# Kernel tuning notes

Measured on AMD Instinct MI355X. Metric: run time of the kernel, lower is better.

Reference implementation:

```python
import jax, jax.numpy as jnp
import numpy as np
from jax import lax

KH, KW, K = 3, 3, 9
PAD, BN_EPS = 1, 1e-5


def setup_inputs() -> dict:
    key = jax.random.key(0)
    ks = jax.random.split(key, 10)
    B, CHI, CHO, H, W = 2, 64, 64, 128, 128
    x = jax.random.normal(ks[0], (B, CHI, H, W), dtype=jnp.float32)
    # offset/mask branch conv: 3*K output channels (o1, o2, mask)
    w_off = jax.random.normal(ks[1], (3 * K, CHI, KH, KW), dtype=jnp.float32) * 0.01
    b_off = jax.random.normal(ks[2], (3 * K,), dtype=jnp.float32) * 0.01
    # main deformable conv weight/bias
    fan = CHI * K
    weight = jax.random.normal(ks[3], (CHO, CHI, KH, KW), dtype=jnp.float32) / np.sqrt(fan)
    bias = jax.random.normal(ks[4], (CHO,), dtype=jnp.float32) * 0.01
    # BatchNorm (eval-mode) params
    gamma = jax.random.uniform(ks[5], (CHO,), minval=0.5, maxval=1.5, dtype=jnp.float32)
    beta = jax.random.normal(ks[6], (CHO,), dtype=jnp.float32) * 0.1
    run_mean = jax.random.normal(ks[7], (CHO,), dtype=jnp.float32) * 0.1
    run_var = jax.random.uniform(ks[8], (CHO,), minval=0.5, maxval=1.5, dtype=jnp.float32)
    return {"x": x, "w_off": w_off, "b_off": b_off, "weight": weight,
            "bias": bias, "gamma": gamma, "beta": beta,
            "run_mean": run_mean, "run_var": run_var}


def _dcn_bn_relu(x, w_off, b_off, weight, bias, gamma, beta, run_mean, run_var):
    B, C, H, W = x.shape
    CHO = weight.shape[0]
    # offset/mask branch: regular 3x3 conv, stride 1, pad 1
    om = lax.conv_general_dilated(
        x, w_off, window_strides=(1, 1), padding=[(PAD, PAD), (PAD, PAD)],
        dimension_numbers=("NCHW", "OIHW", "NCHW")) + b_off[None, :, None, None]
    o1, o2, m = jnp.split(om, 3, axis=1)          # each [B, K, H, W]
    offset = jnp.concatenate([o1, o2], axis=1)    # [B, 2K, H, W]
    off_y = offset[:, 0::2]                       # interleaved (y, x) per tap, as in DCNv2 CUDA
    off_x = offset[:, 1::2]
    mask = jax.nn.sigmoid(m)                      # [B, K, H, W] modulation

    # sampling positions: p = p0 + p_k + offset
    ky, kx = jnp.meshgrid(jnp.arange(KH), jnp.arange(KW), indexing="ij")
    ky = ky.reshape(K).astype(x.dtype)
    kx = kx.reshape(K).astype(x.dtype)
    hh = jnp.arange(H, dtype=x.dtype)
    ww = jnp.arange(W, dtype=x.dtype)
    py = hh[None, None, :, None] - PAD + ky[None, :, None, None] + off_y  # [B,K,H,W]
    px = ww[None, None, None, :] - PAD + kx[None, :, None, None] + off_x

    y0f = jnp.floor(py)
    x0f = jnp.floor(px)
    ly = (py - y0f)[..., None]
    lx = (px - x0f)[..., None]
    y0 = y0f.astype(jnp.int32)
    x0 = x0f.astype(jnp.int32)
    bidx = jnp.arange(B)[:, None, None, None]

    def gather(yi, xi):
        valid = ((yi >= 0) & (yi < H) & (xi >= 0) & (xi < W)).astype(x.dtype)
        yc = jnp.clip(yi, 0, H - 1)
        xc = jnp.clip(xi, 0, W - 1)
        g = x[bidx, :, yc, xc]                    # [B, K, H, W, C]
        return g * valid[..., None]

    v00 = gather(y0, x0)
    v01 = gather(y0, x0 + 1)
    v10 = gather(y0 + 1, x0)
    v11 = gather(y0 + 1, x0 + 1)
    sampled = (v00 * (1 - ly) * (1 - lx) + v01 * (1 - ly) * lx
               + v10 * ly * (1 - lx) + v11 * ly * lx)
    sampled = sampled * mask[..., None]           # modulated

    out = jnp.einsum("bkhwc,ock->bohw", sampled,
                     weight.reshape(CHO, C, K)) + bias[None, :, None, None]

    # eval-mode BatchNorm + ReLU
    inv = gamma / jnp.sqrt(run_var + BN_EPS)
    out = (out - run_mean[None, :, None, None]) * inv[None, :, None, None] \
          + beta[None, :, None, None]
    return jax.nn.relu(out)


def reference(x, w_off, b_off, weight, bias, gamma, beta, run_mean, run_var):
    return _dcn_bn_relu(x, w_off, b_off, weight, bias, gamma, beta, run_mean, run_var)
```

## Files before the change

kernel.cpp:

```cpp
#include <hip/hip_runtime.h>
#include <hip/hip_bf16.h>

#define HH 128
#define WW 128
#define CI 64
#define CO 64
#define SLS 584

typedef __attribute__((ext_vector_type(8))) short short8;
typedef __attribute__((ext_vector_type(4))) float floatx4;

__device__ __forceinline__ unsigned short f2bf(float f) {
  union { float f; unsigned u; } uu; uu.f = f;
  unsigned r = uu.u + 0x7FFFu + ((uu.u >> 16) & 1u);
  return (unsigned short)(r >> 16);
}
__device__ __forceinline__ unsigned pack2bf(float lo, float hi) {
  return (unsigned)f2bf(lo) | ((unsigned)f2bf(hi) << 16);
}

__global__ __launch_bounds__(256) void setup_kernel(
    const float* __restrict__ x, unsigned* __restrict__ xTb,
    const float* __restrict__ weight, const float* __restrict__ bias,
    const float* __restrict__ gamma, const float* __restrict__ beta,
    const float* __restrict__ mean, const float* __restrict__ var,
    const float* __restrict__ w_off, const float* __restrict__ b_off,
    unsigned short* __restrict__ A, unsigned short* __restrict__ w2,
    float* __restrict__ bias2, float* __restrict__ boff2) {
  __shared__ float tile[64][65];
  int bid = blockIdx.x;
  if (bid < 512) {
    int w0 = (bid & 1) * 64;
    int h = (bid >> 1) & (HH - 1);
    int b = bid >> 8;
    int tc = threadIdx.x & 63;
    int tr = threadIdx.x >> 6;
#pragma unroll
    for (int i = 0; i < 16; i++) {
      int c = i * 4 + tr;
      tile[c][tc] = x[((b * CI + c) * HH + h) * WW + w0 + tc];
    }
    __syncthreads();
    int cp = threadIdx.x & 31;
    int wq = threadIdx.x >> 5;
#pragma unroll
    for (int jj = 0; jj < 8; jj++) {
      int wl = jj * 8 + wq;
      unsigned v = pack2bf(tile[2 * cp][wl], tile[2 * cp + 1][wl]);
      xTb[((b * HH + h) * WW + w0 + wl) * 32 + cp] = v;
    }
  } else {
    int idx = (bid - 512) * 256 + threadIdx.x;
    if (idx < 32) boff2[idx] = (idx < 27) ? b_off[idx] : 0.f;
    if (idx < CO * 576) {
      int o = idx / 576, kc = idx - o * 576;
      int k = kc >> 6, c = kc & 63;
      float inv = gamma[o] * rsqrtf(var[o] + 1e-5f);
      A[idx] = f2bf(weight[(o * CI + c) * 9 + k] * inv);
      if (kc == 0) bias2[o] = (bias[o] - mean[o]) * inv + beta[o];
      if (o < 27) w2[idx] = f2bf(w_off[o * 576 + c * 9 + k]);
      else if (o < 32) w2[idx] = 0;
    }
  }
}

__global__ __launch_bounds__(256) void dcn4_kernel(
    const unsigned short* __restrict__ xTb, const unsigned short* __restrict__ w2,
    const float* __restrict__ boff2, const unsigned short* __restrict__ A,
    const float* __restrict__ bias2, float* __restrict__ out) {
  __shared__ __hip_bfloat16 SL[16 * SLS];
  __shared__ float omS[16 * 29];
  __shared__ float4 Pw[144];
  __shared__ int4 Po[144];

  int bid = blockIdx.x;
  int s = bid & 7;
  int n = bid >> 3;
  int b = n >> 7;
  int rem = n & 127;
  int h = s * 16 + (rem >> 3);
  int w0 = (rem & 7) * 16;

  int tid = threadIdx.x;
  int lane = tid & 63;
  int wave = tid >> 6;
  int cp = lane & 31;
  int ph = lane >> 5;
  const unsigned short* xb = xTb + b * (HH * WW * CI);

#pragma unroll
  for (int j = 0; j < 2; j++) {
    int p = wave * 4 + j * 2 + ph;
    int wpx = w0 + p;
#pragma unroll
    for (int dy = 0; dy < 3; dy++) {
      int y = h - 1 + dy;
      bool yok = (unsigned)y < (unsigned)HH;
#pragma unroll
      for (int dx = 0; dx < 3; dx++) {
        int xx = wpx - 1 + dx;
        unsigned v = 0;
        if (yok && (unsigned)xx < (unsigned)WW)
          v = *(const unsigned*)(xb + (y * WW + xx) * CI + 2 * cp);
        *(unsigned*)(&SL[p * SLS + (dy * 3 + dx) * 64 + 2 * cp]) = v;
      }
    }
  }
  __syncthreads();

  int r16 = lane & 15;
  int quad = lane >> 4;

  if (wave < 2) {
    floatx4 t = *(const floatx4*)(boff2 + wave * 16 + quad * 4);
    const unsigned short* ap = w2 + (wave * 16 + r16) * 576 + quad * 8;
    const __hip_bfloat16* bp = &SL[r16 * SLS + quad * 8];
#pragma unroll
    for (int kc0 = 0; kc0 < 576; kc0 += 32) {
      short8 av = *(const short8*)(ap + kc0);
      short8 bv = *(const short8*)(bp + kc0);
      t = __builtin_amdgcn_mfma_f32_16x16x32_bf16(av, bv, t, 0, 0, 0);
    }
#pragma unroll
    for (int r = 0; r < 4; r++) {
      int oc = wave * 16 + quad * 4 + r;
      if (oc < 27) omS[r16 * 29 + oc] = t[r];
    }
  }
  __syncthreads();

  if (lane < 36) {
    int p_loc = (lane * 7282) >> 16;
    int k = lane - p_loc * 9;
    int p = wave * 4 + p_loc;
    const float* ob = omS + p * 29;
    float oy = ob[2 * k], ox = ob[2 * k + 1], mm = ob[18 + k];
    float msk = 1.f / (1.f + __expf(-mm));
    int ky = (k * 11) >> 5;
    int kx = k - 3 * ky;
    float py = (float)(h - 1 + ky) + oy;
    float px = (float)(w0 + p - 1 + kx) + ox;
    float y0f = floorf(py), x0f = floorf(px);
    float ly = py - y0f, lx = px - x0f;
    int y0 = (int)y0f, x0 = (int)x0f;
    int y1 = y0 + 1, x1 = x0 + 1;
    float lylx = ly * lx;
    float w11 = lylx * msk;
    float w10 = (ly - lylx) * msk;
    float w01 = (lx - lylx) * msk;
    float w00 = (1.f - ly - lx + lylx) * msk;
    bool y0v = (unsigned)y0 < (unsigned)HH, y1v = (unsigned)y1 < (unsigned)HH;
    bool x0v = (unsigned)x0 < (unsigned)WW, x1v = (unsigned)x1 < (unsigned)WW;
    int yc0 = min(max(y0, 0), HH - 1), yc1 = min(max(y1, 0), HH - 1);
    int xc0 = min(max(x0, 0), WW - 1), xc1 = min(max(x1, 0), WW - 1);
    Pw[p * 9 + k] = make_float4((y0v && x0v) ? w00 : 0.f, (y0v && x1v) ? w01 : 0.f,
                                (y1v && x0v) ? w10 : 0.f, (y1v && x1v) ? w11 : 0.f);
    Po[p * 9 + k] = make_int4((yc0 * WW + xc0) * CI, (yc0 * WW + xc1) * CI,
                              (yc1 * WW + xc0) * CI, (yc1 * WW + xc1) * CI);
  }

#pragma unroll
  for (int j = 0; j < 2; j++) {
    int p = wave * 4 + j * 2 + ph;
#pragma unroll
    for (int k = 0; k < 9; k++) {
      float4 wv = Pw[p * 9 + k];
      int4 ov = Po[p * 9 + k];
      int ch = 2 * cp;
      unsigned u00 = *(const unsigned*)(xb + ov.x + ch);
      unsigned u01 = *(const unsigned*)(xb + ov.y + ch);
      unsigned u10 = *(const unsigned*)(xb + ov.z + ch);
      unsigned u11 = *(const unsigned*)(xb + ov.w + ch);
      float lo = __uint_as_float(u00 << 16) * wv.x + __uint_as_float(u01 << 16) * wv.y +
                 __uint_as_float(u10 << 16) * wv.z + __uint_as_float(u11 << 16) * wv.w;
      float hi = __uint_as_float(u00 & 0xffff0000u) * wv.x + __uint_as_float(u01 & 0xffff0000u) * wv.y +
                 __uint_as_float(u10 & 0xffff0000u) * wv.z + __uint_as_float(u11 & 0xffff0000u) * wv.w;
      *(unsigned*)(&SL[p * SLS + k * 64 + ch]) = pack2bf(lo, hi);
    }
  }
  __syncthreads();

  floatx4 acc = *(const floatx4*)(bias2 + wave * 16 + quad * 4);
  {
    const unsigned short* Ap = A + (wave * 16 + r16) * 576 + quad * 8;
    const __hip_bfloat16* Sp = &SL[r16 * SLS + quad * 8];
#pragma unroll
    for (int kc0 = 0; kc0 < 576; kc0 += 32) {
      short8 av = *(const short8*)(Ap + kc0);
      short8 bv = *(const short8*)(Sp + kc0);
      acc = __builtin_amdgcn_mfma_f32_16x16x32_bf16(av, bv, acc, 0, 0, 0);
    }
  }
  int p = r16;
#pragma unroll
  for (int r = 0; r < 4; r++) {
    int o = wave * 16 + quad * 4 + r;
    out[((b * CO + o) * HH + h) * WW + w0 + p] = fmaxf(acc[r], 0.f);
  }
}

extern "C" void kernel_launch(void* const* d_in, const int* in_sizes, int n_in,
                              void* d_out, int out_size, void* d_ws, size_t ws_size,
                              hipStream_t stream) {
  const float* x = (const float*)d_in[0];
  const float* w_off = (const float*)d_in[1];
  const float* b_off = (const float*)d_in[2];
  const float* weight = (const float*)d_in[3];
  const float* bias = (const float*)d_in[4];
  const float* gamma = (const float*)d_in[5];
  const float* beta = (const float*)d_in[6];
  const float* run_mean = (const float*)d_in[7];
  const float* run_var = (const float*)d_in[8];
  float* outp = (float*)d_out;

  char* ws = (char*)d_ws;
  unsigned* xTb = (unsigned*)ws;
  unsigned short* A = (unsigned short*)(ws + 4194304);
  unsigned short* w2 = (unsigned short*)(ws + 4268032);
  float* bias2 = (float*)(ws + 4304896);
  float* boff2 = (float*)(ws + 4305152);

  setup_kernel<<<656, 256, 0, stream>>>(x, xTb, weight, bias, gamma, beta,
                                        run_mean, run_var, w_off, b_off,
                                        A, w2, bias2, boff2);
  dcn4_kernel<<<2048, 256, 0, stream>>>((const unsigned short*)xTb, w2, boff2,
                                        A, bias2, outp);
}
```

Before: 115.2 us.

## Split offset conv into row-halo kernel fused with transpose; widen DCN tiles

The offset/mask conv moves into its own kernel. Each block converts a 3-row halo of x to bf16 in shared memory, writes the transposed xTb row, and runs the offset conv from LDS, so the separate transpose pass and the per-tile 3x3 im2col gather from global memory are gone. The main DCN kernel now reads offsets from a global buffer. Each block handles 32 pixels with the main weight fragments held in registers, halving the grid and reusing A across two N-tiles. The cost is an extra global round trip for the offsets, only 256 blocks in the offset kernel, and higher register pressure.

```diff
diff --git a/kernel.cpp b/kernel.cpp
--- a/kernel.cpp
+++ b/kernel.cpp
@@ -6,6 +6,8 @@
 #define CI 64
 #define CO 64
 #define SLS 584
+#define A_HPS 72
+#define A_HW 130
 
 typedef __attribute__((ext_vector_type(8))) short short8;
 typedef __attribute__((ext_vector_type(4))) float floatx4;
@@ -19,121 +21,130 @@
   return (unsigned)f2bf(lo) | ((unsigned)f2bf(hi) << 16);
 }
 
-__global__ __launch_bounds__(256) void setup_kernel(
-    const float* __restrict__ x, unsigned* __restrict__ xTb,
+__global__ __launch_bounds__(256) void prep_kernel(
     const float* __restrict__ weight, const float* __restrict__ bias,
     const float* __restrict__ gamma, const float* __restrict__ beta,
     const float* __restrict__ mean, const float* __restrict__ var,
     const float* __restrict__ w_off, const float* __restrict__ b_off,
-    unsigned short* __restrict__ A, unsigned short* __restrict__ w2,
+    unsigned short* __restrict__ Wm, unsigned short* __restrict__ w2,
     float* __restrict__ bias2, float* __restrict__ boff2) {
-  __shared__ float tile[64][65];
-  int bid = blockIdx.x;
-  if (bid < 512) {
-    int w0 = (bid & 1) * 64;
-    int h = (bid >> 1) & (HH - 1);
-    int b = bid >> 8;
-    int tc = threadIdx.x & 63;
-    int tr = threadIdx.x >> 6;
-#pragma unroll
-    for (int i = 0; i < 16; i++) {
-      int c = i * 4 + tr;
-      tile[c][tc] = x[((b * CI + c) * HH + h) * WW + w0 + tc];
-    }
-    __syncthreads();
-    int cp = threadIdx.x & 31;
-    int wq = threadIdx.x >> 5;
-#pragma unroll
-    for (int jj = 0; jj < 8; jj++) {
-      int wl = jj * 8 + wq;
-      unsigned v = pack2bf(tile[2 * cp][wl], tile[2 * cp + 1][wl]);
-      xTb[((b * HH + h) * WW + w0 + wl) * 32 + cp] = v;
-    }
-  } else {
-    int idx = (bid - 512) * 256 + threadIdx.x;
-    if (idx < 32) boff2[idx] = (idx < 27) ? b_off[idx] : 0.f;
-    if (idx < CO * 576) {
-      int o = idx / 576, kc = idx - o * 576;
-      int k = kc >> 6, c = kc & 63;
-      float inv = gamma[o] * rsqrtf(var[o] + 1e-5f);
-      A[idx] = f2bf(weight[(o * CI + c) * 9 + k] * inv);
-      if (kc == 0) bias2[o] = (bias[o] - mean[o]) * inv + beta[o];
-      if (o < 27) w2[idx] = f2bf(w_off[o * 576 + c * 9 + k]);
-      else if (o < 32) w2[idx] = 0;
-    }
-  }
-}
-
-__global__ __launch_bounds__(256) void dcn4_kernel(
-    const unsigned short* __restrict__ xTb, const unsigned short* __restrict__ w2,
-    const float* __restrict__ boff2, const unsigned short* __restrict__ A,
-    const float* __restrict__ bias2, float* __restrict__ out) {
-  __shared__ __hip_bfloat16 SL[16 * SLS];
-  __shared__ float omS[16 * 29];
-  __shared__ float4 Pw[144];
-  __shared__ int4 Po[144];
-
+  int idx = blockIdx.x * 256 + threadIdx.x;
+  if (idx < 32) boff2[idx] = (idx < 27) ? b_off[idx] : 0.f;
+  if (idx >= CO * 576) return;
+  int o = idx / 576, kc = idx - o * 576;
+  int k = kc >> 6, c = kc & 63;
+  float inv = gamma[o] * rsqrtf(var[o] + 1e-5f);
+  Wm[idx] = f2bf(weight[(o * CI + c) * 9 + k] * inv);
+  if (kc == 0) bias2[o] = (bias[o] - mean[o]) * inv + beta[o];
+  if (o < 27) w2[idx] = f2bf(w_off[o * 576 + c * 9 + k]);
+  else if (o < 32) w2[idx] = 0;
+}
+
+__global__ __launch_bounds__(256) void offA_kernel(
+    const float* __restrict__ x, unsigned* __restrict__ xTb_u,
+    const unsigned short* __restrict__ w2, const float* __restrict__ boff2,
+    float* __restrict__ om32) {
+  __shared__ short halo[3 * A_HW * A_HPS];
   int bid = blockIdx.x;
   int s = bid & 7;
   int n = bid >> 3;
-  int b = n >> 7;
-  int rem = n & 127;
-  int h = s * 16 + (rem >> 3);
-  int w0 = (rem & 7) * 16;
-
+  int b = n >> 4;
+  int h = s * 16 + (n & 15);
   int tid = threadIdx.x;
-  int lane = tid & 63;
-  int wave = tid >> 6;
-  int cp = lane & 31;
-  int ph = lane >> 5;
+  int xx = tid & 127, cg = tid >> 7;
+
+#pragma unroll
+  for (int y3 = 0; y3 < 3; y3++) {
+    int y = h - 1 + y3;
+    bool yok = (unsigned)y < (unsigned)HH;
+    const float* xrow = x + ((long)(b * CI) * HH + y) * WW + xx;
+#pragma unroll
+    for (int cc = 0; cc < 8; cc++) {
+      int c = cg * 32 + cc * 4;
+      float f0 = 0.f, f1 = 0.f, f2 = 0.f, f3 = 0.f;
+      if (yok) {
+        f0 = xrow[(c + 0) * (HH * WW)];
+        f1 = xrow[(c + 1) * (HH * WW)];
+        f2 = xrow[(c + 2) * (HH * WW)];
+        f3 = xrow[(c + 3) * (HH * WW)];
+      }
+      *(uint2*)&halo[(y3 * A_HW + xx + 1) * A_HPS + c] =
+          make_uint2(pack2bf(f0, f1), pack2bf(f2, f3));
+    }
+  }
+  if (tid < 96) {
+    int row = tid >> 5;
+    int rr = tid & 31;
+    int px = (rr >> 4) ? (A_HW - 1) : 0;
+    int q = rr & 15;
+    *(uint2*)&halo[(row * A_HW + px) * A_HPS + q * 4] = make_uint2(0, 0);
+  }
+  __syncthreads();
+
+  {
+    int cp = tid & 31;
+#pragma unroll
+    for (int it = 0; it < 16; it++) {
+      int px = it * 8 + (tid >> 5);
+      unsigned u = *(const unsigned*)&halo[(A_HW + px + 1) * A_HPS + 2 * cp];
+      xTb_u[((b * HH + h) * WW + px) * 32 + cp] = u;
+    }
+  }
+
+  int lane = tid & 63, wave = tid >> 6;
+  int r16 = lane & 15, quad = lane >> 4;
+  int m16 = wave & 1;
+  floatx4 binit = *(const floatx4*)(boff2 + m16 * 16 + quad * 4);
+  const short* ap = (const short*)(w2 + (m16 * 16 + r16) * 576);
+#pragma unroll
+  for (int i = 0; i < 4; i++) {
+    int nt = (wave >> 1) + 2 * i;
+    floatx4 t = binit;
+#pragma unroll
+    for (int kk = 0; kk < 9; kk++) {
+      int dy = kk / 3, dx = kk - 3 * (kk / 3);
+      const short* hp = &halo[(dy * A_HW + nt * 16 + r16 + dx) * A_HPS];
+      short8 b0 = *(const short8*)(hp + quad * 8);
+      short8 b1 = *(const short8*)(hp + 32 + quad * 8);
+      short8 a0 = *(const short8*)(ap + kk * 64 + quad * 8);
+      short8 a1 = *(const short8*)(ap + kk * 64 + 32 + quad * 8);
+      t = __builtin_amdgcn_mfma_f32_16x16x32_bf16(a0, b0, t, 0, 0, 0);
+      t = __builtin_amdgcn_mfma_f32_16x16x32_bf16(a1, b1, t, 0, 0, 0);
+    }
+    float* orow = om32 + (long)(((b * HH + h) * WW) + nt * 16 + r16) * 32;
+#pragma unroll
+    for (int r = 0; r < 4; r++) {
+      int oc = m16 * 16 + quad * 4 + r;
+      if (oc < 27) orow[oc] = t[r];
+    }
+  }
+}
+
+__global__ __launch_bounds__(256) void dcnB_kernel(
+    const unsigned short* __restrict__ xTb, const float* __restrict__ om32,
+    const unsigned short* __restrict__ Wm, const float* __restrict__ bias2,
+    float* __restrict__ out) {
+  __shared__ __hip_bfloat16 SL[32 * SLS];
+  __shared__ float4 Pw[288];
+  __shared__ int4 Po[288];
+
+  int bid = blockIdx.x;
+  int s = bid & 7;
+  int n = bid >> 3;
+  int b = n >> 6;
+  int rem = n & 63;
+  int h = s * 16 + (rem >> 2);
+  int w0 = (rem & 3) * 32;
+
+  int tid = threadIdx.x, lane = tid & 63, wave = tid >> 6;
   const unsigned short* xb = xTb + b * (HH * WW * CI);
-
-#pragma unroll
-  for (int j = 0; j < 2; j++) {
-    int p = wave * 4 + j * 2 + ph;
-    int wpx = w0 + p;
-#pragma unroll
-    for (int dy = 0; dy < 3; dy++) {
-      int y = h - 1 + dy;
-      bool yok = (unsigned)y < (unsigned)HH;
-#pragma unroll
-      for (int dx = 0; dx < 3; dx++) {
-        int xx = wpx - 1 + dx;
-        unsigned v = 0;
-        if (yok && (unsigned)xx < (unsigned)WW)
-          v = *(const unsigned*)(xb + (y * WW + xx) * CI + 2 * cp);
-        *(unsigned*)(&SL[p * SLS + (dy * 3 + dx) * 64 + 2 * cp]) = v;
-      }
-    }
-  }
-  __syncthreads();
-
-  int r16 = lane & 15;
-  int quad = lane >> 4;
-
-  if (wave < 2) {
-    floatx4 t = *(const floatx4*)(boff2 + wave * 16 + quad * 4);
-    const unsigned short* ap = w2 + (wave * 16 + r16) * 576 + quad * 8;
-    const __hip_bfloat16* bp = &SL[r16 * SLS + quad * 8];
-#pragma unroll
-    for (int kc0 = 0; kc0 < 576; kc0 += 32) {
-      short8 av = *(const short8*)(ap + kc0);
-      short8 bv = *(const short8*)(bp + kc0);
-      t = __builtin_amdgcn_mfma_f32_16x16x32_bf16(av, bv, t, 0, 0, 0);
-    }
-#pragma unroll
-    for (int r = 0; r < 4; r++) {
-      int oc = wave * 16 + quad * 4 + r;
-      if (oc < 27) omS[r16 * 29 + oc] = t[r];
-    }
-  }
-  __syncthreads();
-
-  if (lane < 36) {
-    int p_loc = (lane * 7282) >> 16;
-    int k = lane - p_loc * 9;
-    int p = wave * 4 + p_loc;
-    const float* ob = omS + p * 29;
+  int rowpix = (b * HH + h) * WW + w0;
+
+  for (int t2 = lane; t2 < 72; t2 += 64) {
+    int p_loc = (t2 * 7282) >> 16;
+    int k = t2 - p_loc * 9;
+    int p = wave * 8 + p_loc;
+    const float* ob = om32 + (long)(rowpix + p) * 32;
     float oy = ob[2 * k], ox = ob[2 * k + 1], mm = ob[18 + k];
     float msk = 1.f / (1.f + __expf(-mm));
     int ky = (k * 11) >> 5;
@@ -145,28 +156,27 @@
     int y0 = (int)y0f, x0 = (int)x0f;
     int y1 = y0 + 1, x1 = x0 + 1;
     float lylx = ly * lx;
-    float w11 = lylx * msk;
-    float w10 = (ly - lylx) * msk;
-    float w01 = (lx - lylx) * msk;
-    float w00 = (1.f - ly - lx + lylx) * msk;
     bool y0v = (unsigned)y0 < (unsigned)HH, y1v = (unsigned)y1 < (unsigned)HH;
     bool x0v = (unsigned)x0 < (unsigned)WW, x1v = (unsigned)x1 < (unsigned)WW;
     int yc0 = min(max(y0, 0), HH - 1), yc1 = min(max(y1, 0), HH - 1);
     int xc0 = min(max(x0, 0), WW - 1), xc1 = min(max(x1, 0), WW - 1);
-    Pw[p * 9 + k] = make_float4((y0v && x0v) ? w00 : 0.f, (y0v && x1v) ? w01 : 0.f,
-                                (y1v && x0v) ? w10 : 0.f, (y1v && x1v) ? w11 : 0.f);
+    Pw[p * 9 + k] = make_float4((y0v && x0v) ? (1.f - ly - lx + lylx) * msk : 0.f,
+                                (y0v && x1v) ? (lx - lylx) * msk : 0.f,
+                                (y1v && x0v) ? (ly - lylx) * msk : 0.f,
+                                (y1v && x1v) ? lylx * msk : 0.f);
     Po[p * 9 + k] = make_int4((yc0 * WW + xc0) * CI, (yc0 * WW + xc1) * CI,
                               (yc1 * WW + xc0) * CI, (yc1 * WW + xc1) * CI);
   }
 
-#pragma unroll
-  for (int j = 0; j < 2; j++) {
-    int p = wave * 4 + j * 2 + ph;
+  int cp = lane & 31, ph = lane >> 5;
+  int ch = 2 * cp;
+#pragma unroll
+  for (int j = 0; j < 4; j++) {
+    int p = wave * 8 + j * 2 + ph;
 #pragma unroll
     for (int k = 0; k < 9; k++) {
       float4 wv = Pw[p * 9 + k];
       int4 ov = Po[p * 9 + k];
-      int ch = 2 * cp;
       unsigned u00 = *(const unsigned*)(xb + ov.x + ch);
       unsigned u01 = *(const unsigned*)(xb + ov.y + ch);
       unsigned u10 = *(const unsigned*)(xb + ov.z + ch);
@@ -178,24 +188,30 @@
       *(unsigned*)(&SL[p * SLS + k * 64 + ch]) = pack2bf(lo, hi);
     }
   }
+
+  int r16 = lane & 15, quad = lane >> 4;
+  short8 af[18];
+  {
+    const short* Ap = (const short*)(Wm + (wave * 16 + r16) * 576 + quad * 8);
+#pragma unroll
+    for (int i = 0; i < 18; i++) af[i] = *(const short8*)(Ap + 32 * i);
+  }
   __syncthreads();
 
-  floatx4 acc = *(const floatx4*)(bias2 + wave * 16 + quad * 4);
-  {
-    const unsigned short* Ap = A + (wave * 16 + r16) * 576 + quad * 8;
-    const __hip_bfloat16* Sp = &SL[r16 * SLS + quad * 8];
-#pragma unroll
-    for (int kc0 = 0; kc0 < 576; kc0 += 32) {
-      short8 av = *(const short8*)(Ap + kc0);
-      short8 bv = *(const short8*)(Sp + kc0);
-      acc = __builtin_amdgcn_mfma_f32_16x16x32_bf16(av, bv, acc, 0, 0, 0);
-    }
-  }
-  int p = r16;
-#pragma unroll
-  for (int r = 0; r < 4; r++) {
-    int o = wave * 16 + quad * 4 + r;
-    out[((b * CO + o) * HH + h) * WW + w0 + p] = fmaxf(acc[r], 0.f);
+#pragma unroll
+  for (int nt = 0; nt < 2; nt++) {
+    floatx4 acc = *(const floatx4*)(bias2 + wave * 16 + quad * 4);
+    const __hip_bfloat16* Sp = &SL[(nt * 16 + r16) * SLS + quad * 8];
+#pragma unroll
+    for (int i = 0; i < 18; i++) {
+      short8 bv = *(const short8*)(Sp + 32 * i);
+      acc = __builtin_amdgcn_mfma_f32_16x16x32_bf16(af[i], bv, acc, 0, 0, 0);
+    }
+    int o = wave * 16 + quad * 4;
+#pragma unroll
+    for (int r = 0; r < 4; r++) {
+      out[((b * CO + o + r) * HH + h) * WW + w0 + nt * 16 + r16] = fmaxf(acc[r], 0.f);
+    }
   }
 }
 
@@ -215,14 +231,14 @@
 
   char* ws = (char*)d_ws;
   unsigned* xTb = (unsigned*)ws;
-  unsigned short* A = (unsigned short*)(ws + 4194304);
-  unsigned short* w2 = (unsigned short*)(ws + 4268032);
-  float* bias2 = (float*)(ws + 4304896);
-  float* boff2 = (float*)(ws + 4305152);
-
-  setup_kernel<<<656, 256, 0, stream>>>(x, xTb, weight, bias, gamma, beta,
-                                        run_mean, run_var, w_off, b_off,
-                                        A, w2, bias2, boff2);
-  dcn4_kernel<<<2048, 256, 0, stream>>>((const unsigned short*)xTb, w2, boff2,
-                                        A, bias2, outp);
-}
+  float* om32 = (float*)(ws + 4194304);
+  unsigned short* Wm = (unsigned short*)(ws + 8388608);
+  unsigned short* w2 = (unsigned short*)(ws + 8462336);
+  float* bias2 = (float*)(ws + 8499200);
+  float* boff2 = (float*)(ws + 8499456);
+
+  prep_kernel<<<144, 256, 0, stream>>>(weight, bias, gamma, beta, run_mean, run_var,
+                                       w_off, b_off, Wm, w2, bias2, boff2);
+  offA_kernel<<<256, 256, 0, stream>>>(x, xTb, w2, boff2, om32);
+  dcnB_kernel<<<1024, 256, 0, stream>>>((const unsigned short*)xTb, om32, Wm, bias2, outp);
+}
```

Result: faster. 111.1 us (-3.5%).
